# Kernel tuning notes

Hardware: AMD Instinct MI355X
Metric: run time of the kernel (lower is better)

The kernel has to match this reference:

```python
import jax, jax.numpy as jnp
import numpy as np

BETA = 0.25
K = 1024   # codebook_size
D = 64     # emb_dim


def setup_inputs() -> dict:
    key = jax.random.key(0)
    k1, k2 = jax.random.split(key)
    z_e = jax.random.normal(k1, (32, 64, 64, D), dtype=jnp.float32)
    codebook = jax.random.normal(k2, (K, D), dtype=jnp.float32) * 0.05
    return {"z_e": z_e, "codebook": codebook}


def reference(z_e, codebook):
    sg = jax.lax.stop_gradient
    k, d = codebook.shape
    z = z_e.reshape(-1, d)                                   # [N, D]
    # squared euclidean distances: ||z||^2 + ||e||^2 - 2 z.e
    z_sq = jnp.sum(z * z, axis=1, keepdims=True)             # [N, 1]
    e_sq = jnp.sum(codebook * codebook, axis=1)              # [K]
    distances = z_sq + e_sq[None, :] - 2.0 * (z @ codebook.T)  # [N, K]
    indices = jnp.argmin(distances, axis=1)                  # [N] int
    z_q = jnp.take(codebook, indices, axis=0).reshape(z_e.shape)
    commitment = jnp.mean((sg(z_e) - z_q) ** 2)
    codebook_loss = jnp.mean((z_e - sg(z_q)) ** 2)
    z_q_st = z_e + sg(z_q - z_e)
    loss_vq = codebook_loss + BETA * commitment
    # perplexity (no-grad in original)
    n = z.shape[0]
    counts = jnp.zeros((k,), dtype=jnp.float32).at[indices].add(1.0)
    avg_probs = sg(counts / n)
    perplexity = jnp.exp(-jnp.sum(avg_probs * jnp.log(avg_probs + 1e-12)))
    return z_q_st, indices.reshape(z_e.shape[:-1]), loss_vq, perplexity
```

## Files before the change

### kernel.cpp

```cpp
#include <hip/hip_runtime.h>

#define N_VEC   131072
#define D       64
#define KCODES  1024
#define NT      64
#define BLK     256
#define VPB     256
#define CH      4
#define NCH     (NT / CH)

typedef __attribute__((ext_vector_type(8))) short bf16x8;
typedef __attribute__((ext_vector_type(4))) float f32x4;

#define GLD16(dst, src) __builtin_amdgcn_global_load_lds(                      \
    (const __attribute__((address_space(1))) void*)(src),                      \
    (__attribute__((address_space(3))) void*)(dst), 16, 0, 0)


__device__ __forceinline__ float4 f4fma(float4 a, float4 b, float4 c) {
    return make_float4(fmaf(a.x, b.x, c.x), fmaf(a.y, b.y, c.y),
                       fmaf(a.z, b.z, c.z), fmaf(a.w, b.w, c.w));
}
__device__ __forceinline__ float f4rsum(float4 a) {
    return (a.x + a.y) + (a.z + a.w);
}
__device__ __forceinline__ unsigned short f2bf(float f) {
    union { float f; unsigned u; } x; x.f = f;
    unsigned r = x.u + 0x7FFFu + ((x.u >> 16) & 1u);
    return (unsigned short)(r >> 16);
}
__device__ __forceinline__ float bf2f(unsigned short h) {
    union { unsigned u; float f; } x; x.u = ((unsigned)h) << 16;
    return x.f;
}
__device__ __forceinline__ int   f_as_i(float f) { union { float f; int i; } x; x.f = f; return x.i; }
__device__ __forceinline__ float i_as_f(int i)   { union { int i; float f; } x; x.i = i; return x.f; }

__global__ void prep_kernel(const float* __restrict__ cb, float* __restrict__ esq,
                            bf16x8* __restrict__ afrag, float4* __restrict__ efrag) {
    __shared__ float sesq[64];
    const int tid = threadIdx.x;
    const int c0  = blockIdx.x * 64;
    if (tid < 64) {
        const float4* c4 = reinterpret_cast<const float4*>(cb + (size_t)(c0 + tid) * D);
        float4 p = make_float4(0.f, 0.f, 0.f, 0.f);
        #pragma unroll
        for (int i = 0; i < 16; ++i) { float4 v = c4[i]; p = f4fma(v, v, p); }
        float e = f4rsum(p);
        esq[c0 + tid] = e;
        sesq[tid] = e;
    }
    __syncthreads();
    const int tt = tid >> 6;
    const int L  = tid & 63;
    const int t  = blockIdx.x * 4 + tt;
    const int g  = L >> 4;
    const int r  = t * 16 + (L & 15);
    #pragma unroll
    for (int ks = 0; ks < 2; ++ks) {
        const float* src = cb + (size_t)r * D + ks * 32 + g * 8;
        bf16x8 h, l;
        #pragma unroll
        for (int e = 0; e < 8; ++e) {
            float f = src[e];
            unsigned short hb = f2bf(f);
            float lo = f - bf2f(hb);
            h[e] = (short)hb;
            l[e] = (short)f2bf(lo);
        }
        afrag[(t * 4 + ks * 2 + 0) * 64 + L] = h;
        afrag[(t * 4 + ks * 2 + 1) * 64 + L] = l;
    }
    float4 ef;
    ef.x = sesq[tt * 16 + g * 4 + 0];
    ef.y = sesq[tt * 16 + g * 4 + 1];
    ef.z = sesq[tt * 16 + g * 4 + 2];
    ef.w = sesq[tt * 16 + g * 4 + 3];
    efrag[t * 64 + L] = ef;
}

__device__ __forceinline__ void insd(float ov, int og,
                                     float& v0, float& v1, float& v2,
                                     int& g0, int& g1, int& g2) {
    bool b1 = (ov > v0) || (ov == v0 && og < g0);
    bool b2 = (ov > v1) || (ov == v1 && og < g1);
    bool b3 = (ov > v2) || (ov == v2 && og < g2);
    float nv2 = b2 ? v1 : (b3 ? ov : v2);
    int   ng2 = b2 ? g1 : (b3 ? og : g2);
    float nv1 = b1 ? v0 : (b2 ? ov : v1);
    int   ng1 = b1 ? g0 : (b2 ? og : g1);
    v0 = b1 ? ov : v0;
    g0 = b1 ? og : g0;
    v1 = nv1; g1 = ng1; v2 = nv2; g2 = ng2;
}

__launch_bounds__(BLK)
__global__ void vq_fused(const float* __restrict__ z_e, const float* __restrict__ cb,
                         const float* __restrict__ esq,
                         const float4* __restrict__ afrag4, const float4* __restrict__ efrag,
                         float* __restrict__ zq_out, float* __restrict__ idx_out,
                         float* __restrict__ sse, int* __restrict__ counts) {
    __shared__ float4 scb[2][CH * 4 * 64];
    __shared__ float4 sef[2][CH * 64];
    __shared__ float  sred[4];

    const int tid  = threadIdx.x;
    const int wave = tid >> 6;
    const int L    = tid & 63;
    const int lrow = L & 15;
    const int g    = L >> 4;
    const size_t vbase = (size_t)blockIdx.x * VPB + wave * 64;

    bf16x8 zhi[4][2], zlo[4][2];
    #pragma unroll
    for (int b = 0; b < 4; ++b) {
        #pragma unroll
        for (int ks = 0; ks < 2; ++ks) {
            const float* zp = z_e + (vbase + b * 16 + lrow) * D + ks * 32 + g * 8;
            float4 u0 = *reinterpret_cast<const float4*>(zp);
            float4 u1 = *reinterpret_cast<const float4*>(zp + 4);
            float fv[8] = {u0.x, u0.y, u0.z, u0.w, u1.x, u1.y, u1.z, u1.w};
            bf16x8 h, l;
            #pragma unroll
            for (int e = 0; e < 8; ++e) {
                unsigned short hb = f2bf(fv[e]);
                float lo = fv[e] - bf2f(hb);
                h[e] = (short)hb;
                l[e] = (short)f2bf(lo);
            }
            zhi[b][ks] = h; zlo[b][ks] = l;
        }
    }

    float m1[4], m2[4], m3[4];
    #pragma unroll
    for (int b = 0; b < 4; ++b) { m1[b] = m2[b] = m3[b] = -INFINITY; }

    #pragma unroll
    for (int i = 0; i < 4; ++i) GLD16(&scb[0][i * BLK + tid], afrag4 + i * BLK + tid);
    GLD16(&sef[0][tid], efrag + tid);

    int cur = 0;
    for (int c = 0; c < NCH; ++c) {
        __syncthreads();
        if (c + 1 < NCH) {
            const float4* gA = afrag4 + (size_t)(c + 1) * (CH * 4 * 64);
            const float4* gE = efrag + (size_t)(c + 1) * (CH * 64);
            #pragma unroll
            for (int i = 0; i < 4; ++i) GLD16(&scb[cur ^ 1][i * BLK + tid], gA + i * BLK + tid);
            GLD16(&sef[cur ^ 1][tid], gE + tid);
        }

        #pragma unroll
        for (int tt = 0; tt < CH; ++tt) {
            const bf16x8* fr = reinterpret_cast<const bf16x8*>(&scb[cur][tt * 256]);
            bf16x8 Ah0 = fr[0 * 64 + L];
            bf16x8 Al0 = fr[1 * 64 + L];
            bf16x8 Ah1 = fr[2 * 64 + L];
            bf16x8 Al1 = fr[3 * 64 + L];
            float4 ef  = sef[cur][tt * 64 + L];
            const int tglob = c * CH + tt;

            #pragma unroll
            for (int b = 0; b < 4; ++b) {
                f32x4 aA = (f32x4){0.f, 0.f, 0.f, 0.f};
                f32x4 aB = (f32x4){0.f, 0.f, 0.f, 0.f};
                aA = __builtin_amdgcn_mfma_f32_16x16x32_bf16(Ah0, zhi[b][0], aA, 0, 0, 0);
                aB = __builtin_amdgcn_mfma_f32_16x16x32_bf16(Ah0, zlo[b][0], aB, 0, 0, 0);
                aB = __builtin_amdgcn_mfma_f32_16x16x32_bf16(Al0, zhi[b][0], aB, 0, 0, 0);
                aA = __builtin_amdgcn_mfma_f32_16x16x32_bf16(Ah1, zhi[b][1], aA, 0, 0, 0);
                aB = __builtin_amdgcn_mfma_f32_16x16x32_bf16(Ah1, zlo[b][1], aB, 0, 0, 0);
                aB = __builtin_amdgcn_mfma_f32_16x16x32_bf16(Al1, zhi[b][1], aB, 0, 0, 0);

                #pragma unroll
                for (int j = 0; j < 4; ++j) {
                    float ej = (j == 0) ? ef.x : (j == 1) ? ef.y : (j == 2) ? ef.z : ef.w;
                    float s = fmaf(2.0f, aA[j], fmaf(2.0f, aB[j], -ej));
                    int komp = 255 - ((tglob << 2) | j);
                    float pd = i_as_f((f_as_i(s) & 0xFFFFFF00) | komp);
                    float mn = fminf(m2[b], pd);
                    float md = __builtin_amdgcn_fmed3f(m1[b], pd, m2[b]);
                    m1[b] = fmaxf(m1[b], pd);
                    m2[b] = md;
                    m3[b] = fmaxf(m3[b], mn);
                }
            }
        }
        cur ^= 1;
    }

    __syncthreads();

    int (*scand)[3] = reinterpret_cast<int(*)[3]>(&scb[0][0]);
    int*  swin      = reinterpret_cast<int*>(&sef[0][0]);

    #pragma unroll
    for (int b = 0; b < 4; ++b) {
        float v0, v1, v2; int g0, g1, g2;
        {
            int p0 = f_as_i(m1[b]), p1 = f_as_i(m2[b]), p2 = f_as_i(m3[b]);
            int c0 = 255 - (p0 & 255), c1 = 255 - (p1 & 255), c2 = 255 - (p2 & 255);
            v0 = i_as_f(p0 & ~255); g0 = (c0 >> 2) * 16 + g * 4 + (c0 & 3);
            v1 = i_as_f(p1 & ~255); g1 = (c1 >> 2) * 16 + g * 4 + (c1 & 3);
            v2 = i_as_f(p2 & ~255); g2 = (c2 >> 2) * 16 + g * 4 + (c2 & 3);
        }
        #pragma unroll
        for (int m = 16; m <= 32; m <<= 1) {
            float ov0 = __shfl_xor(v0, m), ov1 = __shfl_xor(v1, m), ov2 = __shfl_xor(v2, m);
            int   og0 = __shfl_xor(g0, m), og1 = __shfl_xor(g1, m), og2 = __shfl_xor(g2, m);
            insd(ov0, og0, v0, v1, v2, g0, g1, g2);
            insd(ov1, og1, v0, v1, v2, g0, g1, g2);
            insd(ov2, og2, v0, v1, v2, g0, g1, g2);
        }
        if (g == 0) {
            int lv = wave * 64 + b * 16 + lrow;
            scand[lv][0] = g0; scand[lv][1] = g1; scand[lv][2] = g2;
        }
    }
    __syncthreads();

    const size_t n = (size_t)blockIdx.x * VPB + tid;
    const int ci0 = scand[tid][0];
    const int ci1 = scand[tid][1];
    const int ci2 = scand[tid][2];
    const float4* z4  = reinterpret_cast<const float4*>(z_e + n * D);
    const float4* cp0 = reinterpret_cast<const float4*>(cb + (size_t)ci0 * D);
    const float4* cp1 = reinterpret_cast<const float4*>(cb + (size_t)ci1 * D);
    const float4* cp2 = reinterpret_cast<const float4*>(cb + (size_t)ci2 * D);

    float4 pq = make_float4(0.f, 0.f, 0.f, 0.f);
    float4 s0 = pq, s1 = pq, s2 = pq;
    #pragma unroll
    for (int i = 0; i < 16; ++i) {
        float4 zz = z4[i];
        pq = f4fma(zz, zz, pq);
        s0 = f4fma(zz, cp0[i], s0);
        s1 = f4fma(zz, cp1[i], s1);
        s2 = f4fma(zz, cp2[i], s2);
    }
    const float zsq = f4rsum(pq);

    float bd = INFINITY; int bi = 0x7FFFFFFF;
    {
        float dd = fmaf(-2.0f, f4rsum(s0), zsq + esq[ci0]);
        if (dd < bd || (dd == bd && ci0 < bi)) { bd = dd; bi = ci0; }
    }
    {
        float dd = fmaf(-2.0f, f4rsum(s1), zsq + esq[ci1]);
        if (dd < bd || (dd == bd && ci1 < bi)) { bd = dd; bi = ci1; }
    }
    {
        float dd = fmaf(-2.0f, f4rsum(s2), zsq + esq[ci2]);
        if (dd < bd || (dd == bd && ci2 < bi)) { bd = dd; bi = ci2; }
    }

    idx_out[n] = (float)bi;
    atomicAdd(&counts[bi], 1);
    swin[tid] = bi;

    float v = bd;
    #pragma unroll
    for (int off = 32; off > 0; off >>= 1) v += __shfl_down(v, off);
    if ((tid & 63) == 0) sred[tid >> 6] = v;
    __syncthreads();
    if (tid == 0) atomicAdd(sse, (sred[0] + sred[1]) + (sred[2] + sred[3]));

    const float4* cb4 = reinterpret_cast<const float4*>(cb);
    float4* zq4 = reinterpret_cast<float4*>(zq_out) + (size_t)blockIdx.x * (VPB * 16);
    #pragma unroll
    for (int i = 0; i < 16; ++i) {
        int mi  = i * BLK + tid;
        int vec = mi >> 4;
        int e   = mi & 15;
        zq4[mi] = cb4[(size_t)swin[vec] * 16 + e];
    }
}

__global__ void finalize_kernel(const int* __restrict__ counts, const float* __restrict__ sse,
                                float* __restrict__ out_loss, float* __restrict__ out_perp) {
    __shared__ float red[256];
    int tid = threadIdx.x;
    float hsum = 0.f;
    for (int k = tid; k < KCODES; k += 256) {
        float p = (float)counts[k] / (float)N_VEC;
        hsum += p * logf(p + 1e-12f);
    }
    red[tid] = hsum;
    __syncthreads();
    for (int s = 128; s > 0; s >>= 1) {
        if (tid < s) red[tid] += red[tid + s];
        __syncthreads();
    }
    if (tid == 0) {
        out_loss[0] = 1.25f * sse[0] / 8388608.0f;
        out_perp[0] = expf(-red[0]);
    }
}

extern "C" void kernel_launch(void* const* d_in, const int* in_sizes, int n_in,
                              void* d_out, int out_size, void* d_ws, size_t ws_size,
                              hipStream_t stream) {
    const float* z_e = (const float*)d_in[0];
    const float* cb  = (const float*)d_in[1];

    float* out  = (float*)d_out;
    float* zq   = out;
    float* idxo = out + (size_t)N_VEC * D;
    float* loss = idxo + N_VEC;
    float* perp = loss + 1;

    char* ws = (char*)d_ws;
    int*    counts = (int*)ws;
    float*  sse    = (float*)(ws + 4096);
    float*  esq    = (float*)(ws + 5120);
    float4* efrag  = (float4*)(ws + 16384);
    bf16x8* afrag  = (bf16x8*)(ws + 81920);

    hipMemsetAsync(d_ws, 0, 5120, stream);
    prep_kernel<<<16, 256, 0, stream>>>(cb, esq, afrag, efrag);
    vq_fused<<<N_VEC / VPB, BLK, 0, stream>>>(z_e, cb, esq, (const float4*)afrag, efrag,
                                              zq, idxo, sse, counts);
    finalize_kernel<<<1, 256, 0, stream>>>(counts, sse, loss, perp);
}
```

Before: 115.3 us.

## Split codebook scan across two blocks per tile and rescore candidates in separate kernel

The fused kernel is split in two. vq_main launches twice as many blocks, each scanning half the codebook and writing its top-3 candidate indices packed into one int. A new rescore kernel then evaluates all six candidates exactly in fp32 and writes the outputs. The -0.5*||e||^2 term is folded into the MFMA accumulator init, which removes the separate hi/lo accumulators and the per-element fma. The e-fragment LDS staging is dropped in favour of direct global reads. This raises parallelism and occupancy, at the cost of an extra launch, a candidate buffer round-trip through memory, and re-reading z_e.

```diff
diff --git a/kernel.cpp b/kernel.cpp
--- a/kernel.cpp
+++ b/kernel.cpp
@@ -4,10 +4,11 @@
 #define D       64
 #define KCODES  1024
 #define NT      64
+#define HT      32
 #define BLK     256
 #define VPB     256
 #define CH      4
-#define NCH     (NT / CH)
+#define NCH     (HT / CH)
 
 typedef __attribute__((ext_vector_type(8))) short bf16x8;
 typedef __attribute__((ext_vector_type(4))) float f32x4;
@@ -72,10 +73,10 @@
         afrag[(t * 4 + ks * 2 + 1) * 64 + L] = l;
     }
     float4 ef;
-    ef.x = sesq[tt * 16 + g * 4 + 0];
-    ef.y = sesq[tt * 16 + g * 4 + 1];
-    ef.z = sesq[tt * 16 + g * 4 + 2];
-    ef.w = sesq[tt * 16 + g * 4 + 3];
+    ef.x = -0.5f * sesq[tt * 16 + g * 4 + 0];
+    ef.y = -0.5f * sesq[tt * 16 + g * 4 + 1];
+    ef.z = -0.5f * sesq[tt * 16 + g * 4 + 2];
+    ef.w = -0.5f * sesq[tt * 16 + g * 4 + 3];
     efrag[t * 64 + L] = ef;
 }
 
@@ -95,21 +96,22 @@
 }
 
 __launch_bounds__(BLK)
-__global__ void vq_fused(const float* __restrict__ z_e, const float* __restrict__ cb,
-                         const float* __restrict__ esq,
-                         const float4* __restrict__ afrag4, const float4* __restrict__ efrag,
-                         float* __restrict__ zq_out, float* __restrict__ idx_out,
-                         float* __restrict__ sse, int* __restrict__ counts) {
+__global__ void vq_main(const float* __restrict__ z_e,
+                        const float4* __restrict__ afrag4, const float4* __restrict__ efrag,
+                        int* __restrict__ cand) {
     __shared__ float4 scb[2][CH * 4 * 64];
-    __shared__ float4 sef[2][CH * 64];
-    __shared__ float  sred[4];
 
     const int tid  = threadIdx.x;
     const int wave = tid >> 6;
     const int L    = tid & 63;
     const int lrow = L & 15;
     const int g    = L >> 4;
-    const size_t vbase = (size_t)blockIdx.x * VPB + wave * 64;
+    const int bv   = blockIdx.x >> 1;
+    const int hc   = blockIdx.x & 1;
+    const size_t vbase = (size_t)bv * VPB + wave * 64;
+
+    const float4* afragH = afrag4 + (size_t)hc * (HT * 4 * 64);
+    const float4* efragH = efrag + (size_t)hc * (HT * 64);
 
     bf16x8 zhi[4][2], zlo[4][2];
     #pragma unroll
@@ -137,47 +139,45 @@
     for (int b = 0; b < 4; ++b) { m1[b] = m2[b] = m3[b] = -INFINITY; }
 
     #pragma unroll
-    for (int i = 0; i < 4; ++i) GLD16(&scb[0][i * BLK + tid], afrag4 + i * BLK + tid);
-    GLD16(&sef[0][tid], efrag + tid);
+    for (int i = 0; i < 4; ++i) GLD16(&scb[0][i * BLK + tid], afragH + i * BLK + tid);
 
     int cur = 0;
     for (int c = 0; c < NCH; ++c) {
         __syncthreads();
         if (c + 1 < NCH) {
-            const float4* gA = afrag4 + (size_t)(c + 1) * (CH * 4 * 64);
-            const float4* gE = efrag + (size_t)(c + 1) * (CH * 64);
+            const float4* gA = afragH + (size_t)(c + 1) * (CH * 4 * 64);
             #pragma unroll
             for (int i = 0; i < 4; ++i) GLD16(&scb[cur ^ 1][i * BLK + tid], gA + i * BLK + tid);
-            GLD16(&sef[cur ^ 1][tid], gE + tid);
         }
 
         #pragma unroll
         for (int tt = 0; tt < CH; ++tt) {
+            const int t = c * CH + tt;
             const bf16x8* fr = reinterpret_cast<const bf16x8*>(&scb[cur][tt * 256]);
             bf16x8 Ah0 = fr[0 * 64 + L];
             bf16x8 Al0 = fr[1 * 64 + L];
             bf16x8 Ah1 = fr[2 * 64 + L];
             bf16x8 Al1 = fr[3 * 64 + L];
-            float4 ef  = sef[cur][tt * 64 + L];
-            const int tglob = c * CH + tt;
+            f32x4 einit;
+            {
+                float4 ef = efragH[t * 64 + L];
+                einit[0] = ef.x; einit[1] = ef.y; einit[2] = ef.z; einit[3] = ef.w;
+            }
 
             #pragma unroll
             for (int b = 0; b < 4; ++b) {
-                f32x4 aA = (f32x4){0.f, 0.f, 0.f, 0.f};
-                f32x4 aB = (f32x4){0.f, 0.f, 0.f, 0.f};
-                aA = __builtin_amdgcn_mfma_f32_16x16x32_bf16(Ah0, zhi[b][0], aA, 0, 0, 0);
-                aB = __builtin_amdgcn_mfma_f32_16x16x32_bf16(Ah0, zlo[b][0], aB, 0, 0, 0);
-                aB = __builtin_amdgcn_mfma_f32_16x16x32_bf16(Al0, zhi[b][0], aB, 0, 0, 0);
-                aA = __builtin_amdgcn_mfma_f32_16x16x32_bf16(Ah1, zhi[b][1], aA, 0, 0, 0);
-                aB = __builtin_amdgcn_mfma_f32_16x16x32_bf16(Ah1, zlo[b][1], aB, 0, 0, 0);
-                aB = __builtin_amdgcn_mfma_f32_16x16x32_bf16(Al1, zhi[b][1], aB, 0, 0, 0);
+                f32x4 acc;
+                acc = __builtin_amdgcn_mfma_f32_16x16x32_bf16(Ah0, zhi[b][0], einit, 0, 0, 0);
+                acc = __builtin_amdgcn_mfma_f32_16x16x32_bf16(Ah0, zlo[b][0], acc, 0, 0, 0);
+                acc = __builtin_amdgcn_mfma_f32_16x16x32_bf16(Al0, zhi[b][0], acc, 0, 0, 0);
+                acc = __builtin_amdgcn_mfma_f32_16x16x32_bf16(Ah1, zhi[b][1], acc, 0, 0, 0);
+                acc = __builtin_amdgcn_mfma_f32_16x16x32_bf16(Ah1, zlo[b][1], acc, 0, 0, 0);
+                acc = __builtin_amdgcn_mfma_f32_16x16x32_bf16(Al1, zhi[b][1], acc, 0, 0, 0);
 
                 #pragma unroll
                 for (int j = 0; j < 4; ++j) {
-                    float ej = (j == 0) ? ef.x : (j == 1) ? ef.y : (j == 2) ? ef.z : ef.w;
-                    float s = fmaf(2.0f, aA[j], fmaf(2.0f, aB[j], -ej));
-                    int komp = 255 - ((tglob << 2) | j);
-                    float pd = i_as_f((f_as_i(s) & 0xFFFFFF00) | komp);
+                    int komp = 255 - ((t << 2) | j);
+                    float pd = i_as_f((f_as_i(acc[j]) & 0xFFFFFF00) | komp);
                     float mn = fminf(m2[b], pd);
                     float md = __builtin_amdgcn_fmed3f(m1[b], pd, m2[b]);
                     m1[b] = fmaxf(m1[b], pd);
@@ -189,20 +189,16 @@
         cur ^= 1;
     }
 
-    __syncthreads();
-
-    int (*scand)[3] = reinterpret_cast<int(*)[3]>(&scb[0][0]);
-    int*  swin      = reinterpret_cast<int*>(&sef[0][0]);
-
+    const int cbase = hc * (HT * 16);
     #pragma unroll
     for (int b = 0; b < 4; ++b) {
         float v0, v1, v2; int g0, g1, g2;
         {
             int p0 = f_as_i(m1[b]), p1 = f_as_i(m2[b]), p2 = f_as_i(m3[b]);
             int c0 = 255 - (p0 & 255), c1 = 255 - (p1 & 255), c2 = 255 - (p2 & 255);
-            v0 = i_as_f(p0 & ~255); g0 = (c0 >> 2) * 16 + g * 4 + (c0 & 3);
-            v1 = i_as_f(p1 & ~255); g1 = (c1 >> 2) * 16 + g * 4 + (c1 & 3);
-            v2 = i_as_f(p2 & ~255); g2 = (c2 >> 2) * 16 + g * 4 + (c2 & 3);
+            v0 = i_as_f(p0 & ~255); g0 = cbase + (c0 >> 2) * 16 + g * 4 + (c0 & 3);
+            v1 = i_as_f(p1 & ~255); g1 = cbase + (c1 >> 2) * 16 + g * 4 + (c1 & 3);
+            v2 = i_as_f(p2 & ~255); g2 = cbase + (c2 >> 2) * 16 + g * 4 + (c2 & 3);
         }
         #pragma unroll
         for (int m = 16; m <= 32; m <<= 1) {
@@ -213,45 +209,52 @@
             insd(ov2, og2, v0, v1, v2, g0, g1, g2);
         }
         if (g == 0) {
-            int lv = wave * 64 + b * 16 + lrow;
-            scand[lv][0] = g0; scand[lv][1] = g1; scand[lv][2] = g2;
-        }
-    }
-    __syncthreads();
-
-    const size_t n = (size_t)blockIdx.x * VPB + tid;
-    const int ci0 = scand[tid][0];
-    const int ci1 = scand[tid][1];
-    const int ci2 = scand[tid][2];
-    const float4* z4  = reinterpret_cast<const float4*>(z_e + n * D);
-    const float4* cp0 = reinterpret_cast<const float4*>(cb + (size_t)ci0 * D);
-    const float4* cp1 = reinterpret_cast<const float4*>(cb + (size_t)ci1 * D);
-    const float4* cp2 = reinterpret_cast<const float4*>(cb + (size_t)ci2 * D);
+            size_t n = vbase + b * 16 + lrow;
+            cand[(size_t)hc * N_VEC + n] = (g0 & 1023) | ((g1 & 1023) << 10) | ((g2 & 1023) << 20);
+        }
+    }
+}
+
+__launch_bounds__(256)
+__global__ void rescore_kernel(const float* __restrict__ z_e, const float* __restrict__ cb,
+                               const float* __restrict__ esq, const int* __restrict__ cand,
+                               float* __restrict__ zq_out, float* __restrict__ idx_out,
+                               float* __restrict__ sse, int* __restrict__ counts) {
+    __shared__ int   swin[256];
+    __shared__ float sred[4];
+    const int tid = threadIdx.x;
+    const size_t n = (size_t)blockIdx.x * 256 + tid;
+
+    const int p0 = cand[n];
+    const int p1 = cand[N_VEC + n];
+    int ci[6];
+    ci[0] = p0 & 1023; ci[1] = (p0 >> 10) & 1023; ci[2] = (p0 >> 20) & 1023;
+    ci[3] = p1 & 1023; ci[4] = (p1 >> 10) & 1023; ci[5] = (p1 >> 20) & 1023;
+
+    const float4* z4 = reinterpret_cast<const float4*>(z_e + n * D);
+    const float4* cp[6];
+    #pragma unroll
+    for (int k = 0; k < 6; ++k) cp[k] = reinterpret_cast<const float4*>(cb + (size_t)ci[k] * D);
 
     float4 pq = make_float4(0.f, 0.f, 0.f, 0.f);
-    float4 s0 = pq, s1 = pq, s2 = pq;
+    float4 s[6];
+    #pragma unroll
+    for (int k = 0; k < 6; ++k) s[k] = pq;
     #pragma unroll
     for (int i = 0; i < 16; ++i) {
         float4 zz = z4[i];
         pq = f4fma(zz, zz, pq);
-        s0 = f4fma(zz, cp0[i], s0);
-        s1 = f4fma(zz, cp1[i], s1);
-        s2 = f4fma(zz, cp2[i], s2);
+        #pragma unroll
+        for (int k = 0; k < 6; ++k) s[k] = f4fma(zz, cp[k][i], s[k]);
     }
     const float zsq = f4rsum(pq);
 
     float bd = INFINITY; int bi = 0x7FFFFFFF;
-    {
-        float dd = fmaf(-2.0f, f4rsum(s0), zsq + esq[ci0]);
-        if (dd < bd || (dd == bd && ci0 < bi)) { bd = dd; bi = ci0; }
-    }
-    {
-        float dd = fmaf(-2.0f, f4rsum(s1), zsq + esq[ci1]);
-        if (dd < bd || (dd == bd && ci1 < bi)) { bd = dd; bi = ci1; }
-    }
-    {
-        float dd = fmaf(-2.0f, f4rsum(s2), zsq + esq[ci2]);
-        if (dd < bd || (dd == bd && ci2 < bi)) { bd = dd; bi = ci2; }
+    #pragma unroll
+    for (int k = 0; k < 6; ++k) {
+        float t1 = zsq + esq[ci[k]];
+        float dd = fmaf(-2.0f, f4rsum(s[k]), t1);
+        if (dd < bd || (dd == bd && ci[k] < bi)) { bd = dd; bi = ci[k]; }
     }
 
     idx_out[n] = (float)bi;
@@ -266,10 +269,10 @@
     if (tid == 0) atomicAdd(sse, (sred[0] + sred[1]) + (sred[2] + sred[3]));
 
     const float4* cb4 = reinterpret_cast<const float4*>(cb);
-    float4* zq4 = reinterpret_cast<float4*>(zq_out) + (size_t)blockIdx.x * (VPB * 16);
+    float4* zq4 = reinterpret_cast<float4*>(zq_out) + (size_t)blockIdx.x * (256 * 16);
     #pragma unroll
     for (int i = 0; i < 16; ++i) {
-        int mi  = i * BLK + tid;
+        int mi  = i * 256 + tid;
         int vec = mi >> 4;
         int e   = mi & 15;
         zq4[mi] = cb4[(size_t)swin[vec] * 16 + e];
@@ -315,10 +318,11 @@
     float*  esq    = (float*)(ws + 5120);
     float4* efrag  = (float4*)(ws + 16384);
     bf16x8* afrag  = (bf16x8*)(ws + 81920);
+    int*    cand   = (int*)(ws + 344064);
 
     hipMemsetAsync(d_ws, 0, 5120, stream);
     prep_kernel<<<16, 256, 0, stream>>>(cb, esq, afrag, efrag);
-    vq_fused<<<N_VEC / VPB, BLK, 0, stream>>>(z_e, cb, esq, (const float4*)afrag, efrag,
-                                              zq, idxo, sse, counts);
+    vq_main<<<(N_VEC / VPB) * 2, BLK, 0, stream>>>(z_e, (const float4*)afrag, efrag, cand);
+    rescore_kernel<<<N_VEC / 256, 256, 0, stream>>>(z_e, cb, esq, cand, zq, idxo, sse, counts);
     finalize_kernel<<<1, 256, 0, stream>>>(counts, sse, loss, perp);
 }
```

Measured after the change: 142.5 us. 1.24x slower.

## Halve vectors per block, fold esq into MFMA accumulator, split rescoring across threads

Applied to the files above, without the earlier changes.

Each block now handles 128 vectors instead of 256. Each wave tracks 2 row-blocks instead of 4, so the grid has twice as many blocks. The codebook norm term is pre-scaled by -0.5 and used as the MFMA accumulator's initial value. This merges the two accumulator chains into one and removes the per-element fma work when building candidate scores. The exact fp32 rescoring of the three candidates is split across two threads per vector and combined through LDS. The cost is extra barriers, and the codebook fragments are streamed from global memory to LDS once per block, so doubling the block count doubles that traffic.

```diff
diff --git a/kernel.cpp b/kernel.cpp
--- a/kernel.cpp
+++ b/kernel.cpp
@@ -5,7 +5,7 @@
 #define KCODES  1024
 #define NT      64
 #define BLK     256
-#define VPB     256
+#define VPB     128
 #define CH      4
 #define NCH     (NT / CH)
 
@@ -72,10 +72,10 @@
         afrag[(t * 4 + ks * 2 + 1) * 64 + L] = l;
     }
     float4 ef;
-    ef.x = sesq[tt * 16 + g * 4 + 0];
-    ef.y = sesq[tt * 16 + g * 4 + 1];
-    ef.z = sesq[tt * 16 + g * 4 + 2];
-    ef.w = sesq[tt * 16 + g * 4 + 3];
+    ef.x = -0.5f * sesq[tt * 16 + g * 4 + 0];
+    ef.y = -0.5f * sesq[tt * 16 + g * 4 + 1];
+    ef.z = -0.5f * sesq[tt * 16 + g * 4 + 2];
+    ef.w = -0.5f * sesq[tt * 16 + g * 4 + 3];
     efrag[t * 64 + L] = ef;
 }
 
@@ -102,18 +102,24 @@
                          float* __restrict__ sse, int* __restrict__ counts) {
     __shared__ float4 scb[2][CH * 4 * 64];
     __shared__ float4 sef[2][CH * 64];
-    __shared__ float  sred[4];
+    char* ovl = (char*)&scb[0][0];
+    int  (*scand)[3] = reinterpret_cast<int(*)[3]>(ovl);
+    float* sZsq = reinterpret_cast<float*>(ovl + 2048);
+    float* sS1  = reinterpret_cast<float*>(ovl + 2560);
+    float* sS2  = reinterpret_cast<float*>(ovl + 3072);
+    float* sC2  = reinterpret_cast<float*>(ovl + 3584);
+    float* sred = reinterpret_cast<float*>(ovl + 4096);
 
     const int tid  = threadIdx.x;
     const int wave = tid >> 6;
     const int L    = tid & 63;
     const int lrow = L & 15;
     const int g    = L >> 4;
-    const size_t vbase = (size_t)blockIdx.x * VPB + wave * 64;
-
-    bf16x8 zhi[4][2], zlo[4][2];
-    #pragma unroll
-    for (int b = 0; b < 4; ++b) {
+    const size_t vbase = (size_t)blockIdx.x * VPB + wave * 32;
+
+    bf16x8 zhi[2][2], zlo[2][2];
+    #pragma unroll
+    for (int b = 0; b < 2; ++b) {
         #pragma unroll
         for (int ks = 0; ks < 2; ++ks) {
             const float* zp = z_e + (vbase + b * 16 + lrow) * D + ks * 32 + g * 8;
@@ -132,9 +138,9 @@
         }
     }
 
-    float m1[4], m2[4], m3[4];
-    #pragma unroll
-    for (int b = 0; b < 4; ++b) { m1[b] = m2[b] = m3[b] = -INFINITY; }
+    float m1[2], m2[2], m3[2];
+    #pragma unroll
+    for (int b = 0; b < 2; ++b) { m1[b] = m2[b] = m3[b] = -INFINITY; }
 
     #pragma unroll
     for (int i = 0; i < 4; ++i) GLD16(&scb[0][i * BLK + tid], afrag4 + i * BLK + tid);
@@ -153,31 +159,32 @@
 
         #pragma unroll
         for (int tt = 0; tt < CH; ++tt) {
+            const int t = c * CH + tt;
             const bf16x8* fr = reinterpret_cast<const bf16x8*>(&scb[cur][tt * 256]);
             bf16x8 Ah0 = fr[0 * 64 + L];
             bf16x8 Al0 = fr[1 * 64 + L];
             bf16x8 Ah1 = fr[2 * 64 + L];
             bf16x8 Al1 = fr[3 * 64 + L];
-            float4 ef  = sef[cur][tt * 64 + L];
-            const int tglob = c * CH + tt;
-
-            #pragma unroll
-            for (int b = 0; b < 4; ++b) {
-                f32x4 aA = (f32x4){0.f, 0.f, 0.f, 0.f};
-                f32x4 aB = (f32x4){0.f, 0.f, 0.f, 0.f};
-                aA = __builtin_amdgcn_mfma_f32_16x16x32_bf16(Ah0, zhi[b][0], aA, 0, 0, 0);
-                aB = __builtin_amdgcn_mfma_f32_16x16x32_bf16(Ah0, zlo[b][0], aB, 0, 0, 0);
-                aB = __builtin_amdgcn_mfma_f32_16x16x32_bf16(Al0, zhi[b][0], aB, 0, 0, 0);
-                aA = __builtin_amdgcn_mfma_f32_16x16x32_bf16(Ah1, zhi[b][1], aA, 0, 0, 0);
-                aB = __builtin_amdgcn_mfma_f32_16x16x32_bf16(Ah1, zlo[b][1], aB, 0, 0, 0);
-                aB = __builtin_amdgcn_mfma_f32_16x16x32_bf16(Al1, zhi[b][1], aB, 0, 0, 0);
+            f32x4 einit;
+            {
+                float4 ef = sef[cur][tt * 64 + L];
+                einit[0] = ef.x; einit[1] = ef.y; einit[2] = ef.z; einit[3] = ef.w;
+            }
+
+            #pragma unroll
+            for (int b = 0; b < 2; ++b) {
+                f32x4 acc;
+                acc = __builtin_amdgcn_mfma_f32_16x16x32_bf16(Ah0, zhi[b][0], einit, 0, 0, 0);
+                acc = __builtin_amdgcn_mfma_f32_16x16x32_bf16(Ah0, zlo[b][0], acc, 0, 0, 0);
+                acc = __builtin_amdgcn_mfma_f32_16x16x32_bf16(Al0, zhi[b][0], acc, 0, 0, 0);
+                acc = __builtin_amdgcn_mfma_f32_16x16x32_bf16(Ah1, zhi[b][1], acc, 0, 0, 0);
+                acc = __builtin_amdgcn_mfma_f32_16x16x32_bf16(Ah1, zlo[b][1], acc, 0, 0, 0);
+                acc = __builtin_amdgcn_mfma_f32_16x16x32_bf16(Al1, zhi[b][1], acc, 0, 0, 0);
 
                 #pragma unroll
                 for (int j = 0; j < 4; ++j) {
-                    float ej = (j == 0) ? ef.x : (j == 1) ? ef.y : (j == 2) ? ef.z : ef.w;
-                    float s = fmaf(2.0f, aA[j], fmaf(2.0f, aB[j], -ej));
-                    int komp = 255 - ((tglob << 2) | j);
-                    float pd = i_as_f((f_as_i(s) & 0xFFFFFF00) | komp);
+                    int komp = 255 - ((t << 2) | j);
+                    float pd = i_as_f((f_as_i(acc[j]) & 0xFFFFFF00) | komp);
                     float mn = fminf(m2[b], pd);
                     float md = __builtin_amdgcn_fmed3f(m1[b], pd, m2[b]);
                     m1[b] = fmaxf(m1[b], pd);
@@ -191,11 +198,8 @@
 
     __syncthreads();
 
-    int (*scand)[3] = reinterpret_cast<int(*)[3]>(&scb[0][0]);
-    int*  swin      = reinterpret_cast<int*>(&sef[0][0]);
-
-    #pragma unroll
-    for (int b = 0; b < 4; ++b) {
+    #pragma unroll
+    for (int b = 0; b < 2; ++b) {
         float v0, v1, v2; int g0, g1, g2;
         {
             int p0 = f_as_i(m1[b]), p1 = f_as_i(m2[b]), p2 = f_as_i(m3[b]);
@@ -213,52 +217,64 @@
             insd(ov2, og2, v0, v1, v2, g0, g1, g2);
         }
         if (g == 0) {
-            int lv = wave * 64 + b * 16 + lrow;
+            int lv = wave * 32 + b * 16 + lrow;
             scand[lv][0] = g0; scand[lv][1] = g1; scand[lv][2] = g2;
         }
     }
     __syncthreads();
 
-    const size_t n = (size_t)blockIdx.x * VPB + tid;
-    const int ci0 = scand[tid][0];
-    const int ci1 = scand[tid][1];
-    const int ci2 = scand[tid][2];
-    const float4* z4  = reinterpret_cast<const float4*>(z_e + n * D);
-    const float4* cp0 = reinterpret_cast<const float4*>(cb + (size_t)ci0 * D);
-    const float4* cp1 = reinterpret_cast<const float4*>(cb + (size_t)ci1 * D);
-    const float4* cp2 = reinterpret_cast<const float4*>(cb + (size_t)ci2 * D);
-
-    float4 pq = make_float4(0.f, 0.f, 0.f, 0.f);
-    float4 s0 = pq, s1 = pq, s2 = pq;
-    #pragma unroll
-    for (int i = 0; i < 16; ++i) {
-        float4 zz = z4[i];
-        pq = f4fma(zz, zz, pq);
-        s0 = f4fma(zz, cp0[i], s0);
-        s1 = f4fma(zz, cp1[i], s1);
-        s2 = f4fma(zz, cp2[i], s2);
-    }
-    const float zsq = f4rsum(pq);
-
-    float bd = INFINITY; int bi = 0x7FFFFFFF;
+    const int vid = tid & (VPB - 1);
+    const int sub = tid >> 7;
+    const size_t n = (size_t)blockIdx.x * VPB + vid;
     {
-        float dd = fmaf(-2.0f, f4rsum(s0), zsq + esq[ci0]);
-        if (dd < bd || (dd == bd && ci0 < bi)) { bd = dd; bi = ci0; }
-    }
-    {
-        float dd = fmaf(-2.0f, f4rsum(s1), zsq + esq[ci1]);
-        if (dd < bd || (dd == bd && ci1 < bi)) { bd = dd; bi = ci1; }
-    }
-    {
-        float dd = fmaf(-2.0f, f4rsum(s2), zsq + esq[ci2]);
-        if (dd < bd || (dd == bd && ci2 < bi)) { bd = dd; bi = ci2; }
-    }
-
-    idx_out[n] = (float)bi;
-    atomicAdd(&counts[bi], 1);
-    swin[tid] = bi;
-
-    float v = bd;
+        const float4* z4 = reinterpret_cast<const float4*>(z_e + n * D);
+        if (sub == 0) {
+            int ci0 = scand[vid][0];
+            const float4* cp0 = reinterpret_cast<const float4*>(cb + (size_t)ci0 * D);
+            float4 pq = make_float4(0.f, 0.f, 0.f, 0.f);
+            float4 s0 = pq;
+            #pragma unroll
+            for (int i = 0; i < 16; ++i) {
+                float4 zz = z4[i];
+                pq = f4fma(zz, zz, pq);
+                s0 = f4fma(zz, cp0[i], s0);
+            }
+            sZsq[vid] = f4rsum(pq);
+            sS1[vid]  = f4rsum(s0);
+        } else {
+            int ci1 = scand[vid][1];
+            int ci2 = scand[vid][2];
+            const float4* cp1 = reinterpret_cast<const float4*>(cb + (size_t)ci1 * D);
+            const float4* cp2 = reinterpret_cast<const float4*>(cb + (size_t)ci2 * D);
+            float4 s1 = make_float4(0.f, 0.f, 0.f, 0.f);
+            float4 s2 = s1;
+            #pragma unroll
+            for (int i = 0; i < 16; ++i) {
+                float4 zz = z4[i];
+                s1 = f4fma(zz, cp1[i], s1);
+                s2 = f4fma(zz, cp2[i], s2);
+            }
+            sS2[vid] = f4rsum(s1);
+            sC2[vid] = f4rsum(s2);
+        }
+    }
+    __syncthreads();
+
+    float v = 0.f;
+    if (sub == 0) {
+        int ci0 = scand[vid][0], ci1 = scand[vid][1], ci2 = scand[vid][2];
+        float zsq = sZsq[vid];
+        float d0 = fmaf(-2.0f, sS1[vid], zsq + esq[ci0]);
+        float d1 = fmaf(-2.0f, sS2[vid], zsq + esq[ci1]);
+        float d2 = fmaf(-2.0f, sC2[vid], zsq + esq[ci2]);
+        float bd = d0; int bi = ci0;
+        if (d1 < bd || (d1 == bd && ci1 < bi)) { bd = d1; bi = ci1; }
+        if (d2 < bd || (d2 == bd && ci2 < bi)) { bd = d2; bi = ci2; }
+        idx_out[n] = (float)bi;
+        atomicAdd(&counts[bi], 1);
+        scand[vid][0] = bi;
+        v = bd;
+    }
     #pragma unroll
     for (int off = 32; off > 0; off >>= 1) v += __shfl_down(v, off);
     if ((tid & 63) == 0) sred[tid >> 6] = v;
@@ -268,11 +284,11 @@
     const float4* cb4 = reinterpret_cast<const float4*>(cb);
     float4* zq4 = reinterpret_cast<float4*>(zq_out) + (size_t)blockIdx.x * (VPB * 16);
     #pragma unroll
-    for (int i = 0; i < 16; ++i) {
+    for (int i = 0; i < 8; ++i) {
         int mi  = i * BLK + tid;
         int vec = mi >> 4;
         int e   = mi & 15;
-        zq4[mi] = cb4[(size_t)swin[vec] * 16 + e];
+        zq4[mi] = cb4[(size_t)scand[vec][0] * 16 + e];
     }
 }
 
```

Result: faster. 103.7 us, median of 2 (-10.0%).
